# Optimization experiments

Measured on AMD Instinct MI355X. Metric: run time of the kernel, lower is better.

## Reference

```python
import jax, jax.numpy as jnp
from jax import lax
import numpy as np

N_WORDS, SENT_LEN, N_HEADS = 8192, 64, 1024
INPUT_SIZE, HIDDEN, DIST_EMB, CONV_CH, MAX_DIST = 768, 1024, 64, 4, 128
L_MAX = SENT_LEN  # static max sentence length (uniform sentences in setup)


def setup_inputs():
    key = jax.random.key(0)
    ks = jax.random.split(key, 8)
    sent_id = (jnp.arange(N_WORDS) // SENT_LEN).astype(jnp.int32)
    words = jax.random.normal(ks[0], (N_WORDS, INPUT_SIZE), jnp.float32)
    heads_ids = jnp.sort(jax.random.randint(ks[1], (N_HEADS,), 0, N_WORDS)).astype(jnp.int32)
    in_dim = 2 * INPUT_SIZE + DIST_EMB
    def lin(k, i, o):
        return (jax.random.normal(k, (i, o), jnp.float32) / np.float32(np.sqrt(i)))
    return dict(
        sent_id=sent_id, words=words, heads_ids=heads_ids,
        W1=lin(ks[2], in_dim, HIDDEN), b1=jnp.zeros((HIDDEN,), jnp.float32),
        W2=lin(ks[3], HIDDEN, 256), b2=jnp.zeros((256,), jnp.float32),
        W3=lin(ks[4], 256, DIST_EMB), b3=jnp.zeros((DIST_EMB,), jnp.float32),
        conv1_w=jax.random.normal(ks[5], (CONV_CH, DIST_EMB, 3), jnp.float32) * 0.05,
        conv1_b=jnp.zeros((CONV_CH,), jnp.float32),
        conv2_w=jax.random.normal(ks[6], (2, CONV_CH, 3), jnp.float32) * 0.2,
        conv2_b=jnp.zeros((2,), jnp.float32),
        emb=jax.random.normal(ks[7], (MAX_DIST, DIST_EMB), jnp.float32),
    )


def _conv1d(x, w, b):
    # x: [N, C_in, L], w: [C_out, C_in, K=3]; padding=1 exactly as the torch module
    y = lax.conv_general_dilated(x, w, (1,), [(1, 1)],
                                 dimension_numbers=('NCH', 'OIH', 'NCH'))
    return y + b[None, :, None]


def reference(sent_id, words, heads_ids, W1, b1, W2, b2, W3, b3,
              conv1_w, conv1_b, conv2_w, conv2_b, emb):
    n_words = words.shape[0]
    n_heads = heads_ids.shape[0]
    md = emb.shape[0]
    heads = heads_ids.astype(jnp.int32)
    sid_h = sent_id[heads]
    # sent_id is sorted: each sentence is a contiguous run of words, so the
    # ragged nonzero(same_sent) cols for head h are start[h] .. start[h]+len[h]-1
    start = jnp.searchsorted(sent_id, sid_h, side='left')
    lengths = jnp.searchsorted(sent_id, sid_h, side='right') - start
    j = jnp.arange(L_MAX)
    cols = start[:, None] + j[None, :]                  # [H, L]
    valid = j[None, :] < lengths[:, None]               # padding_mask
    cols_c = jnp.minimum(cols, n_words - 1)
    rel = heads[:, None] - cols_c                       # relative positions
    emb_ids = rel + (md - 2) // 2
    emb_ids = jnp.where((emb_ids < 0) | (emb_ids > md - 2), md - 1, emb_ids)
    # padded pair matrix: [H, L, 2*input + dist_emb], zeros at padded slots
    pair = jnp.concatenate([
        jnp.broadcast_to(words[heads][:, None, :], (n_heads, L_MAX, words.shape[1])),
        words[cols_c],
        emb[emb_ids],
    ], axis=-1)
    pair = jnp.where(valid[..., None], pair, 0.0)
    # FFNN (eval mode: dropout = identity)
    h = jax.nn.relu(pair @ W1 + b1)
    h = jax.nn.relu(h @ W2 + b2)
    h = h @ W3 + b3                                     # [H, L, DIST_EMB]
    x = jnp.transpose(h, (0, 2, 1))                     # [H, C, L]
    x = _conv1d(x, conv1_w, conv1_b)
    x = _conv1d(x, conv2_w, conv2_b)
    res = jnp.transpose(x, (0, 2, 1))                   # [H, L, 2]
    # scatter valid entries back into a -inf-filled [H, n_words, 2] tensor
    scores = jnp.full((n_heads, n_words, 2), -jnp.inf, jnp.float32)
    rows = jnp.broadcast_to(jnp.arange(n_heads)[:, None], cols.shape)
    cols_sc = jnp.where(valid, cols, n_words)           # OOB index -> dropped
    scores = scores.at[rows, cols_sc].set(res, mode='drop')
    # eval-mode validity masks: starts must be <= head, ends >= head
    rel_full = heads[:, None] - jnp.arange(n_words)[None, :]
    valid_starts = jnp.where(rel_full >= 0, 0.0, -jnp.inf)
    valid_ends = jnp.where(rel_full <= 0, 0.0, -jnp.inf)
    return scores + jnp.stack([valid_starts, valid_ends], axis=2)
```

## Files before the change

### kernel.cpp

```cpp
#include <hip/hip_runtime.h>
#include <cstdint>
#include <cstddef>

#define NW   8192
#define NH   1024
#define INP  768
#define HID  1024
#define DE   64
#define LMAX 64

#define NEG_SENT (-3.0e38f)

typedef short bf16x8 __attribute__((ext_vector_type(8)));
typedef float f32x4  __attribute__((ext_vector_type(4)));

__device__ __forceinline__ unsigned short f2bf(float f) {
    unsigned u = __builtin_bit_cast(unsigned, f);
    u += 0x7FFFu + ((u >> 16) & 1u);
    return (unsigned short)(u >> 16);
}
__device__ __forceinline__ float bcf(unsigned u) {
    return __builtin_bit_cast(float, u);
}

__device__ __forceinline__ void gload_lds16(const void* g, void* lds) {
    __builtin_amdgcn_global_load_lds(
        (const __attribute__((address_space(1))) unsigned int*)g,
        (__attribute__((address_space(3))) unsigned int*)lds, 16, 0, 0);
}

__device__ __forceinline__ bf16x8 mk_af(uint4 u, uint4 v, uint4 e) {
    bf16x8 r;
    const unsigned* up = (const unsigned*)&u;
    const unsigned* vp = (const unsigned*)&v;
    const unsigned* ep = (const unsigned*)&e;
    unsigned* rp = (unsigned*)&r;
    #pragma unroll
    for (int q = 0; q < 4; ++q) {
        const unsigned ud = up[q], vd = vp[q], ed = ep[q];
        float slo = bcf(ud << 16) + bcf(vd << 16) + bcf(ed << 16);
        float shi = bcf(ud & 0xffff0000u) + bcf(vd & 0xffff0000u) + bcf(ed & 0xffff0000u);
        slo = fmaxf(slo, 0.f);
        shi = fmaxf(shi, 0.f);
        rp[q] = (unsigned)f2bf(slo) | ((unsigned)f2bf(shi) << 16);
    }
    return r;
}

__device__ __forceinline__ void pack_frags_body(
    const float* __restrict__ src, uint4* __restrict__ dst,
    int Ntiles, int N, int t)
{
    const int frag = t >> 6, l = t & 63;
    const int kc = frag / Ntiles, nt = frag - kc * Ntiles;
    const int k0 = kc * 32 + ((l >> 4) << 3);
    const int n  = nt * 16 + (l & 15);
    unsigned wv[4];
    #pragma unroll
    for (int r = 0; r < 4; ++r) {
        const unsigned lo = f2bf(src[(size_t)(k0 + 2 * r)     * N + n]);
        const unsigned hi = f2bf(src[(size_t)(k0 + 2 * r + 1) * N + n]);
        wv[r] = lo | (hi << 16);
    }
    dst[t] = make_uint4(wv[0], wv[1], wv[2], wv[3]);
}

__device__ __forceinline__ void pack_rows_body(
    const float* __restrict__ src, uint4* __restrict__ dst,
    const int* __restrict__ gather, int Kc, int ldsrc, int t)
{
    const int l = t & 63, frag = t >> 6;
    const int mt = frag / Kc, kc = frag - mt * Kc;
    int row = mt * 16 + (l & 15);
    if (gather) row = gather[row];
    const int k0 = kc * 32 + ((l >> 4) << 3);
    const float* s = src + (size_t)row * ldsrc + k0;
    unsigned wv[4];
    #pragma unroll
    for (int r = 0; r < 4; ++r) {
        const unsigned lo = f2bf(s[2 * r]);
        const unsigned hi = f2bf(s[2 * r + 1]);
        wv[r] = lo | (hi << 16);
    }
    dst[t] = make_uint4(wv[0], wv[1], wv[2], wv[3]);
}

__global__ __launch_bounds__(256) void pack_all(
    const int* __restrict__ sent_id, const int* __restrict__ heads_ids,
    const float* __restrict__ W1, const float* __restrict__ b1,
    const float* __restrict__ W2, const float* __restrict__ W3,
    const float* __restrict__ words, const float* __restrict__ emb,
    uint4* __restrict__ W2p, uint4* __restrict__ W3p,
    uint4* __restrict__ W1bp, uint4* __restrict__ W1ap,
    uint4* __restrict__ W1cp, uint4* __restrict__ Ep_a,
    uint4* __restrict__ Awp, uint4* __restrict__ Aup,
    unsigned short* __restrict__ b1b, unsigned short* __restrict__ zrow,
    int* __restrict__ hstart, int* __restrict__ hlen)
{
    const int b = blockIdx.x, tid = threadIdx.x;
    if (b < 4) {
        const int i = b * 256 + tid;
        b1b[i] = f2bf(b1[i]);
        zrow[i] = 0;
        const int head = heads_ids[i];
        const int sid = sent_id[head];
        int lo = 0, hi = NW;
        while (lo < hi) { int m = (lo + hi) >> 1; if (sent_id[m] < sid) lo = m + 1; else hi = m; }
        const int st = lo;
        int lo2 = lo, hi2 = NW;
        while (lo2 < hi2) { int m = (lo2 + hi2) >> 1; if (sent_id[m] <= sid) lo2 = m + 1; else hi2 = m; }
        int ln = lo2 - st;
        if (ln > LMAX) ln = LMAX;
        hstart[i] = st; hlen[i] = ln;
    }
    else if (b < 132)  pack_frags_body(W2, W2p, 16, 256, (b - 4) * 256 + tid);
    else if (b < 140)  pack_frags_body(W3, W3p, 4, 64, (b - 132) * 256 + tid);
    else if (b < 524)  pack_frags_body(W1 + (size_t)INP * HID, W1bp, 64, 1024, (b - 140) * 256 + tid);
    else if (b < 908)  pack_frags_body(W1, W1ap, 64, 1024, (b - 524) * 256 + tid);
    else if (b < 940)  pack_frags_body(W1 + (size_t)2 * INP * HID, W1cp, 64, 1024, (b - 908) * 256 + tid);
    else if (b < 4012) pack_rows_body(words, Awp, nullptr, 24, INP, (b - 940) * 256 + tid);
    else if (b < 4396) pack_rows_body(words, Aup, heads_ids, 24, INP, (b - 4012) * 256 + tid);
    else               pack_rows_body(emb, Ep_a, nullptr, 2, DE, (b - 4396) * 256 + tid);
}

__global__ __launch_bounds__(256) void gemm_vue(
    const uint4* __restrict__ Awp, const uint4* __restrict__ W1bp,
    const uint4* __restrict__ Aup, const uint4* __restrict__ W1ap,
    const uint4* __restrict__ Ep_a, const uint4* __restrict__ W1cp,
    const float* __restrict__ b1,
    unsigned short* __restrict__ Vb, unsigned short* __restrict__ Ub,
    unsigned short* __restrict__ Eb)
{
    __shared__ uint4 sAB[2][1024];
    const int tid = threadIdx.x;
    const int l = tid & 63, wid = tid >> 6;

    const uint4 *Ap, *Bp;
    unsigned short* Cb;
    const float* bias = nullptr;
    int Kc, by, bx;
    {
        const int bid = blockIdx.x;
        if (bid < 512)      { Ap = Awp;  Bp = W1bp; Cb = Vb; Kc = 24; by = bid >> 3; bx = bid & 7; }
        else if (bid < 576) { const int bb = bid - 512; Ap = Aup; Bp = W1ap; Cb = Ub; bias = b1; Kc = 24; by = bb >> 3; bx = bb & 7; }
        else                { const int bb = bid - 576; Ap = Ep_a; Bp = W1cp; Cb = Eb; Kc = 2; by = 0; bx = bb; }
    }
    const int mt0 = by * 8, nt0 = bx * 8;
    const int NtTot = 64, N = 1024;
    const int wm = (wid >> 1) * 4, wn = (wid & 1) * 4;

    f32x4 acc[4][4];
    #pragma unroll
    for (int i = 0; i < 4; ++i)
        #pragma unroll
        for (int j = 0; j < 4; ++j) acc[i][j] = (f32x4){0.f, 0.f, 0.f, 0.f};

    #pragma unroll
    for (int i = 0; i < 2; ++i) {
        const int f = i * 4 + wid;
        gload_lds16(Ap + (size_t)(mt0 + f) * Kc * 64 + l, &sAB[0][f * 64 + l]);
        gload_lds16(Bp + (size_t)(nt0 + f) * 64 + l,      &sAB[0][(8 + f) * 64 + l]);
    }

    for (int kc = 0; kc < Kc; ++kc) {
        const int p = kc & 1;
        __builtin_amdgcn_s_barrier();
        if (kc + 1 < Kc) {
            #pragma unroll
            for (int i = 0; i < 2; ++i) {
                const int f = i * 4 + wid;
                gload_lds16(Ap + ((size_t)(mt0 + f) * Kc + kc + 1) * 64 + l,
                            &sAB[p ^ 1][f * 64 + l]);
                gload_lds16(Bp + ((size_t)(kc + 1) * NtTot + nt0 + f) * 64 + l,
                            &sAB[p ^ 1][(8 + f) * 64 + l]);
            }
            asm volatile("s_waitcnt vmcnt(4)" ::: "memory");
        } else {
            asm volatile("s_waitcnt vmcnt(0)" ::: "memory");
        }
        __builtin_amdgcn_s_barrier();
        bf16x8 af[4], bf[4];
        #pragma unroll
        for (int i = 0; i < 4; ++i)
            af[i] = *(const bf16x8*)&sAB[p][(wm + i) * 64 + l];
        #pragma unroll
        for (int j = 0; j < 4; ++j)
            bf[j] = *(const bf16x8*)&sAB[p][(8 + wn + j) * 64 + l];
        #pragma unroll
        for (int i = 0; i < 4; ++i)
            #pragma unroll
            for (int j = 0; j < 4; ++j)
                acc[i][j] = __builtin_amdgcn_mfma_f32_16x16x32_bf16(
                    af[i], bf[j], acc[i][j], 0, 0, 0);
    }
    const int bm = mt0 * 16, bn = nt0 * 16;
    #pragma unroll
    for (int i = 0; i < 4; ++i)
        #pragma unroll
        for (int j = 0; j < 4; ++j) {
            const int row0 = bm + (wm + i) * 16 + ((l >> 4) << 2);
            const int col  = bn + (wn + j) * 16 + (l & 15);
            const float bv = bias ? bias[col] : 0.f;
            #pragma unroll
            for (int r = 0; r < 4; ++r)
                Cb[(size_t)(row0 + r) * N + col] = f2bf(acc[i][j][r] + bv);
        }
}

__global__ __launch_bounds__(256, 3) void head_kernel(
    const int* __restrict__ hstart, const int* __restrict__ hlen,
    const int* __restrict__ heads_ids,
    const unsigned short* __restrict__ Vb, const unsigned short* __restrict__ Ub,
    const unsigned short* __restrict__ Eb, const unsigned short* __restrict__ b1b,
    const unsigned short* __restrict__ zrow,
    const uint4* __restrict__ W2p, const float* __restrict__ b2,
    const uint4* __restrict__ W3p, const float* __restrict__ b3,
    const float* __restrict__ c1w, const float* __restrict__ c1b,
    const float* __restrict__ c2w, const float* __restrict__ c2b,
    float* __restrict__ out)
{
    __shared__ char smem[50464];
    const int h   = blockIdx.x;
    const int tid = threadIdx.x;
    const int w = tid >> 6, l = tid & 63;
    const int head  = heads_ids[h];
    const int start = hstart[h];
    const int len   = hlen[h];

    const int arow = w * 16 + (l & 15);
    const int g8   = (l >> 4) << 3;
    const bool valid = arow < len;
    const int wglob = start + arow;
    const int wc    = wglob < NW ? wglob : NW - 1;
    int eid = head - wc + 63;
    eid = (eid < 0 || eid > 126) ? 127 : eid;
    const unsigned short* Up = valid ? Ub + (size_t)h   * HID : b1b;
    const unsigned short* Vp = valid ? Vb + (size_t)wc  * HID : zrow;
    const unsigned short* Ep = valid ? Eb + (size_t)eid * HID : zrow;

    char* slot0 = smem;
    char* slot1 = smem + 4096;
    char* myA   = smem + w * 1024 + l * 16;
    const uint4* WpB = W2p + (size_t)(w * 4) * 64 + l;

    f32x4 acc[16];
    #pragma unroll
    for (int i = 0; i < 16; ++i) acc[i] = (f32x4){0.f, 0.f, 0.f, 0.f};

    uint4 uA, vA, eA, uB, vB, eB;
    bf16x8 Ba0, Ba1, Ba2, Ba3, Bb0, Bb1, Bb2, Bb3;

    #define LOAD_AGL(kc, uu, vv, ee) do {                      \
        uu = *(const uint4*)(Up + (kc) * 32 + g8);             \
        vv = *(const uint4*)(Vp + (kc) * 32 + g8);             \
        ee = *(const uint4*)(Ep + (kc) * 32 + g8); } while (0)
    #define LOAD_B(kc, b0, b1v, b2v, b3v) do {                 \
        const uint4* p_ = WpB + (size_t)(kc) * 16 * 64;        \
        b0  = *(const bf16x8*)(p_);                            \
        b1v = *(const bf16x8*)(p_ + 64);                       \
        b2v = *(const bf16x8*)(p_ + 128);                      \
        b3v = *(const bf16x8*)(p_ + 192); } while (0)
    #define CONSUME(slot, b0, b1v, b2v, b3v) do {              \
        bf16x8 a0 = *(const bf16x8*)((slot) + 0 * 1024 + l * 16); \
        bf16x8 a1 = *(const bf16x8*)((slot) + 1 * 1024 + l * 16); \
        bf16x8 a2 = *(const bf16x8*)((slot) + 2 * 1024 + l * 16); \
        bf16x8 a3 = *(const bf16x8*)((slot) + 3 * 1024 + l * 16); \
        acc[0]  = __builtin_amdgcn_mfma_f32_16x16x32_bf16(a0, b0,  acc[0],  0,0,0); \
        acc[1]  = __builtin_amdgcn_mfma_f32_16x16x32_bf16(a0, b1v, acc[1],  0,0,0); \
        acc[2]  = __builtin_amdgcn_mfma_f32_16x16x32_bf16(a0, b2v, acc[2],  0,0,0); \
        acc[3]  = __builtin_amdgcn_mfma_f32_16x16x32_bf16(a0, b3v, acc[3],  0,0,0); \
        acc[4]  = __builtin_amdgcn_mfma_f32_16x16x32_bf16(a1, b0,  acc[4],  0,0,0); \
        acc[5]  = __builtin_amdgcn_mfma_f32_16x16x32_bf16(a1, b1v, acc[5],  0,0,0); \
        acc[6]  = __builtin_amdgcn_mfma_f32_16x16x32_bf16(a1, b2v, acc[6],  0,0,0); \
        acc[7]  = __builtin_amdgcn_mfma_f32_16x16x32_bf16(a1, b3v, acc[7],  0,0,0); \
        acc[8]  = __builtin_amdgcn_mfma_f32_16x16x32_bf16(a2, b0,  acc[8],  0,0,0); \
        acc[9]  = __builtin_amdgcn_mfma_f32_16x16x32_bf16(a2, b1v, acc[9],  0,0,0); \
        acc[10] = __builtin_amdgcn_mfma_f32_16x16x32_bf16(a2, b2v, acc[10], 0,0,0); \
        acc[11] = __builtin_amdgcn_mfma_f32_16x16x32_bf16(a2, b3v, acc[11], 0,0,0); \
        acc[12] = __builtin_amdgcn_mfma_f32_16x16x32_bf16(a3, b0,  acc[12], 0,0,0); \
        acc[13] = __builtin_amdgcn_mfma_f32_16x16x32_bf16(a3, b1v, acc[13], 0,0,0); \
        acc[14] = __builtin_amdgcn_mfma_f32_16x16x32_bf16(a3, b2v, acc[14], 0,0,0); \
        acc[15] = __builtin_amdgcn_mfma_f32_16x16x32_bf16(a3, b3v, acc[15], 0,0,0); } while (0)

    LOAD_AGL(0, uA, vA, eA);
    LOAD_B(0, Ba0, Ba1, Ba2, Ba3);
    LOAD_AGL(1, uB, vB, eB);
    LOAD_B(1, Bb0, Bb1, Bb2, Bb3);
    {
        bf16x8 af = mk_af(uA, vA, eA);
        *(bf16x8*)(slot0 + w * 1024 + l * 16) = af;
    }
    LOAD_AGL(2, uA, vA, eA);

    for (int kc = 0; kc < 32; kc += 2) {
        __builtin_amdgcn_s_barrier();
        {
            bf16x8 af = mk_af(uB, vB, eB);
            *(bf16x8*)(slot1 + w * 1024 + l * 16) = af;
        }
        if (kc + 3 < 32) LOAD_AGL(kc + 3, uB, vB, eB);
        CONSUME(slot0, Ba0, Ba1, Ba2, Ba3);
        if (kc + 2 < 32) LOAD_B(kc + 2, Ba0, Ba1, Ba2, Ba3);
        __builtin_amdgcn_s_barrier();
        if (kc + 2 < 32) {
            bf16x8 af = mk_af(uA, vA, eA);
            *(bf16x8*)(slot0 + w * 1024 + l * 16) = af;
        }
        if (kc + 4 < 32) LOAD_AGL(kc + 4, uA, vA, eA);
        CONSUME(slot1, Bb0, Bb1, Bb2, Bb3);
        if (kc + 3 < 32) LOAD_B(kc + 3, Bb0, Bb1, Bb2, Bb3);
    }
    #undef LOAD_AGL
    #undef LOAD_B
    #undef CONSUME
    (void)myA;

    __syncthreads();
    {
        float b2v[4];
        #pragma unroll
        for (int ntl = 0; ntl < 4; ++ntl) b2v[ntl] = b2[w * 64 + ntl * 16 + (l & 15)];
        #pragma unroll
        for (int mt = 0; mt < 4; ++mt)
            #pragma unroll
            for (int ntl = 0; ntl < 4; ++ntl) {
                const int n = w * 64 + ntl * 16 + (l & 15);
                #pragma unroll
                for (int r = 0; r < 4; ++r) {
                    const int m = mt * 16 + ((l >> 4) << 2) + r;
                    const float x = fmaxf(acc[mt * 4 + ntl][r] + b2v[ntl], 0.f);
                    *(unsigned short*)(smem + m * 512 + ((n * 2) ^ ((m & 7) << 4))) = f2bf(x);
                }
            }
    }
    __syncthreads();

    f32x4 acc3[4];
    #pragma unroll
    for (int i = 0; i < 4; ++i) acc3[i] = (f32x4){0.f, 0.f, 0.f, 0.f};
    const int mrow = w * 16 + (l & 15);
    #pragma unroll
    for (int kc = 0; kc < 8; ++kc) {
        const int n0 = kc * 32 + g8;
        const bf16x8 af = *(const bf16x8*)(smem + mrow * 512 + ((n0 * 2) ^ ((mrow & 7) << 4)));
        #pragma unroll
        for (int nt = 0; nt < 4; ++nt) {
            const bf16x8 bf = *(const bf16x8*)(W3p + (size_t)((kc << 2) + nt) * 64 + l);
            acc3[nt] = __builtin_amdgcn_mfma_f32_16x16x32_bf16(af, bf, acc3[nt], 0, 0, 0);
        }
    }
    float* h3s = (float*)(smem + 32768);
    float* o1  = (float*)(smem + 32768 + 16640);
    #pragma unroll
    for (int nt = 0; nt < 4; ++nt) {
        const int c = nt * 16 + (l & 15);
        const float b3v = b3[c];
        #pragma unroll
        for (int r = 0; r < 4; ++r) {
            const int m = w * 16 + ((l >> 4) << 2) + r;
            h3s[m * 65 + c] = acc3[nt][r] + b3v;
        }
    }
    if (tid < 8) o1[(tid >> 1) * 66 + ((tid & 1) ? 65 : 0)] = 0.f;
    __syncthreads();

    {
        const int o = tid >> 6, ll = tid & 63;
        float a = c1b[o];
        #pragma unroll 8
        for (int cc = 0; cc < 64; ++cc) {
            const float w0  = c1w[o * 192 + cc * 3 + 0];
            const float w1  = c1w[o * 192 + cc * 3 + 1];
            const float w2v = c1w[o * 192 + cc * 3 + 2];
            if (ll > 0)  a += h3s[(ll - 1) * 65 + cc] * w0;
            a += h3s[ll * 65 + cc] * w1;
            if (ll < 63) a += h3s[(ll + 1) * 65 + cc] * w2v;
        }
        o1[o * 66 + ll + 1] = a;
    }
    __syncthreads();

    if (tid < 128) {
        const int s = tid >> 6, ll = tid & 63;
        float z = c2b[s];
        #pragma unroll
        for (int cc = 0; cc < 4; ++cc)
            #pragma unroll
            for (int k = 0; k < 3; ++k)
                z += o1[cc * 66 + ll + k] * c2w[s * 12 + cc * 3 + k];
        if (ll < len) {
            const int wv = start + ll;
            const bool ok = (s == 0) ? (wv <= head) : (wv >= head);
            out[(size_t)h * (NW * 2) + (size_t)wv * 2 + s] = ok ? z : NEG_SENT;
        }
    }

    {
        float4 ni; ni.x = NEG_SENT; ni.y = NEG_SENT; ni.z = NEG_SENT; ni.w = NEG_SENT;
        float4* orow = reinterpret_cast<float4*>(out + (size_t)h * (NW * 2));
        const int cA = start >> 1;
        const int cB = (start + len - 1) >> 1;
        for (int ch = tid; ch < NW / 2; ch += 256) {
            if (ch >= cA && ch <= cB) {
                #pragma unroll
                for (int t = 0; t < 2; ++t) {
                    const int wv = 2 * ch + t;
                    if (wv < start || wv >= start + len) {
                        out[(size_t)h * (NW * 2) + (size_t)wv * 2]     = NEG_SENT;
                        out[(size_t)h * (NW * 2) + (size_t)wv * 2 + 1] = NEG_SENT;
                    }
                }
            } else {
                orow[ch] = ni;
            }
        }
    }
}

extern "C" void kernel_launch(void* const* d_in, const int* in_sizes, int n_in,
                              void* d_out, int out_size, void* d_ws, size_t ws_size,
                              hipStream_t stream)
{
    const int*   sent_id = (const int*)  d_in[0];
    const float* words   = (const float*)d_in[1];
    const int*   heads   = (const int*)  d_in[2];
    const float* W1      = (const float*)d_in[3];
    const float* b1      = (const float*)d_in[4];
    const float* W2      = (const float*)d_in[5];
    const float* b2      = (const float*)d_in[6];
    const float* W3      = (const float*)d_in[7];
    const float* b3      = (const float*)d_in[8];
    const float* c1w     = (const float*)d_in[9];
    const float* c1b     = (const float*)d_in[10];
    const float* c2w     = (const float*)d_in[11];
    const float* c2b     = (const float*)d_in[12];
    const float* emb     = (const float*)d_in[13];
    float* out = (float*)d_out;

    uint4* W2p  = (uint4*)d_ws;
    uint4* W3p  = W2p  + 32 * 16 * 64;
    uint4* W1bp = W3p  + 8 * 4 * 64;
    uint4* W1ap = W1bp + 24 * 64 * 64;
    uint4* W1cp = W1ap + 24 * 64 * 64;
    uint4* Ep_a = W1cp + 2 * 64 * 64;
    uint4* Awp  = Ep_a + 8 * 2 * 64;
    uint4* Aup  = Awp  + 512 * 24 * 64;
    unsigned short* Vb   = (unsigned short*)(Aup + 64 * 24 * 64);
    unsigned short* Ub   = Vb + (size_t)NW * HID;
    unsigned short* Eb   = Ub + (size_t)NH * HID;
    unsigned short* b1b  = Eb + (size_t)128 * HID;
    unsigned short* zrow = b1b + HID;
    int* hstart = (int*)(zrow + HID);
    int* hlen   = hstart + NH;

    dim3 blk(256);
    pack_all<<<dim3(4400), blk, 0, stream>>>(
        sent_id, heads, W1, b1, W2, W3, words, emb,
        W2p, W3p, W1bp, W1ap, W1cp, Ep_a, Awp, Aup, b1b, zrow, hstart, hlen);
    gemm_vue<<<dim3(584), blk, 0, stream>>>(
        Awp, W1bp, Aup, W1ap, Ep_a, W1cp, b1, Vb, Ub, Eb);
    head_kernel<<<dim3(NH), blk, 0, stream>>>(
        hstart, hlen, heads, Vb, Ub, Eb, b1b, zrow,
        W2p, b2, W3p, b3, c1w, c1b, c2w, c2b, out);
}
```

Before: 234.8 us.

## Fuse activation bf16 packing into GEMM and shrink head kernel LDS

```diff
diff --git a/kernel.cpp b/kernel.cpp
--- a/kernel.cpp
+++ b/kernel.cpp
@@ -44,6 +44,15 @@
         shi = fmaxf(shi, 0.f);
         rp[q] = (unsigned)f2bf(slo) | ((unsigned)f2bf(shi) << 16);
     }
+    return r;
+}
+
+__device__ __forceinline__ bf16x8 cvt8(float4 x, float4 y) {
+    bf16x8 r;
+    r[0] = (short)f2bf(x.x); r[1] = (short)f2bf(x.y);
+    r[2] = (short)f2bf(x.z); r[3] = (short)f2bf(x.w);
+    r[4] = (short)f2bf(y.x); r[5] = (short)f2bf(y.y);
+    r[6] = (short)f2bf(y.z); r[7] = (short)f2bf(y.w);
     return r;
 }
 
@@ -65,35 +74,13 @@
     dst[t] = make_uint4(wv[0], wv[1], wv[2], wv[3]);
 }
 
-__device__ __forceinline__ void pack_rows_body(
-    const float* __restrict__ src, uint4* __restrict__ dst,
-    const int* __restrict__ gather, int Kc, int ldsrc, int t)
-{
-    const int l = t & 63, frag = t >> 6;
-    const int mt = frag / Kc, kc = frag - mt * Kc;
-    int row = mt * 16 + (l & 15);
-    if (gather) row = gather[row];
-    const int k0 = kc * 32 + ((l >> 4) << 3);
-    const float* s = src + (size_t)row * ldsrc + k0;
-    unsigned wv[4];
-    #pragma unroll
-    for (int r = 0; r < 4; ++r) {
-        const unsigned lo = f2bf(s[2 * r]);
-        const unsigned hi = f2bf(s[2 * r + 1]);
-        wv[r] = lo | (hi << 16);
-    }
-    dst[t] = make_uint4(wv[0], wv[1], wv[2], wv[3]);
-}
-
 __global__ __launch_bounds__(256) void pack_all(
     const int* __restrict__ sent_id, const int* __restrict__ heads_ids,
     const float* __restrict__ W1, const float* __restrict__ b1,
     const float* __restrict__ W2, const float* __restrict__ W3,
-    const float* __restrict__ words, const float* __restrict__ emb,
     uint4* __restrict__ W2p, uint4* __restrict__ W3p,
     uint4* __restrict__ W1bp, uint4* __restrict__ W1ap,
-    uint4* __restrict__ W1cp, uint4* __restrict__ Ep_a,
-    uint4* __restrict__ Awp, uint4* __restrict__ Aup,
+    uint4* __restrict__ W1cp,
     unsigned short* __restrict__ b1b, unsigned short* __restrict__ zrow,
     int* __restrict__ hstart, int* __restrict__ hlen)
 {
@@ -117,75 +104,89 @@
     else if (b < 140)  pack_frags_body(W3, W3p, 4, 64, (b - 132) * 256 + tid);
     else if (b < 524)  pack_frags_body(W1 + (size_t)INP * HID, W1bp, 64, 1024, (b - 140) * 256 + tid);
     else if (b < 908)  pack_frags_body(W1, W1ap, 64, 1024, (b - 524) * 256 + tid);
-    else if (b < 940)  pack_frags_body(W1 + (size_t)2 * INP * HID, W1cp, 64, 1024, (b - 908) * 256 + tid);
-    else if (b < 4012) pack_rows_body(words, Awp, nullptr, 24, INP, (b - 940) * 256 + tid);
-    else if (b < 4396) pack_rows_body(words, Aup, heads_ids, 24, INP, (b - 4012) * 256 + tid);
-    else               pack_rows_body(emb, Ep_a, nullptr, 2, DE, (b - 4396) * 256 + tid);
+    else               pack_frags_body(W1 + (size_t)2 * INP * HID, W1cp, 64, 1024, (b - 908) * 256 + tid);
 }
 
 __global__ __launch_bounds__(256) void gemm_vue(
-    const uint4* __restrict__ Awp, const uint4* __restrict__ W1bp,
-    const uint4* __restrict__ Aup, const uint4* __restrict__ W1ap,
-    const uint4* __restrict__ Ep_a, const uint4* __restrict__ W1cp,
-    const float* __restrict__ b1,
+    const float* __restrict__ words, const int* __restrict__ heads_ids,
+    const float* __restrict__ emb,
+    const uint4* __restrict__ W1bp, const uint4* __restrict__ W1ap,
+    const uint4* __restrict__ W1cp, const float* __restrict__ b1,
     unsigned short* __restrict__ Vb, unsigned short* __restrict__ Ub,
     unsigned short* __restrict__ Eb)
 {
-    __shared__ uint4 sAB[2][1024];
+    __shared__ char sbuf[2][16384];
     const int tid = threadIdx.x;
     const int l = tid & 63, wid = tid >> 6;
 
-    const uint4 *Ap, *Bp;
-    unsigned short* Cb;
-    const float* bias = nullptr;
-    int Kc, by, bx;
+    const float* Asrc; const int* gather = nullptr;
+    const uint4* Bp; unsigned short* Cb; const float* bias = nullptr;
+    int Kc, by, bx, lda;
     {
         const int bid = blockIdx.x;
-        if (bid < 512)      { Ap = Awp;  Bp = W1bp; Cb = Vb; Kc = 24; by = bid >> 3; bx = bid & 7; }
-        else if (bid < 576) { const int bb = bid - 512; Ap = Aup; Bp = W1ap; Cb = Ub; bias = b1; Kc = 24; by = bb >> 3; bx = bb & 7; }
-        else                { const int bb = bid - 576; Ap = Ep_a; Bp = W1cp; Cb = Eb; Kc = 2; by = 0; bx = bb; }
+        if (bid < 512)      { Asrc = words; lda = INP; Bp = W1bp; Cb = Vb; Kc = 24; by = bid >> 3; bx = bid & 7; }
+        else if (bid < 576) { const int bb = bid - 512; Asrc = words; lda = INP; gather = heads_ids; Bp = W1ap; Cb = Ub; bias = b1; Kc = 24; by = bb >> 3; bx = bb & 7; }
+        else                { const int bb = bid - 576; Asrc = emb; lda = DE; Bp = W1cp; Cb = Eb; Kc = 2; by = 0; bx = bb; }
     }
     const int mt0 = by * 8, nt0 = bx * 8;
     const int NtTot = 64, N = 1024;
     const int wm = (wid >> 1) * 4, wn = (wid & 1) * 4;
 
+    const float* arow[2]; int koffA[2];
+    #pragma unroll
+    for (int q = 0; q < 2; ++q) {
+        const int e = tid + q * 256;
+        const int f = e >> 6, ll2 = e & 63;
+        int r = (mt0 + f) * 16 + (ll2 & 15);
+        if (gather) r = gather[r];
+        arow[q]  = Asrc + (size_t)r * lda;
+        koffA[q] = (ll2 >> 4) << 3;
+    }
+
     f32x4 acc[4][4];
     #pragma unroll
     for (int i = 0; i < 4; ++i)
         #pragma unroll
         for (int j = 0; j < 4; ++j) acc[i][j] = (f32x4){0.f, 0.f, 0.f, 0.f};
 
-    #pragma unroll
-    for (int i = 0; i < 2; ++i) {
-        const int f = i * 4 + wid;
-        gload_lds16(Ap + (size_t)(mt0 + f) * Kc * 64 + l, &sAB[0][f * 64 + l]);
-        gload_lds16(Bp + (size_t)(nt0 + f) * 64 + l,      &sAB[0][(8 + f) * 64 + l]);
-    }
+    float4 a0, a1, a2, a3;
+    #define STAGE_A_LOAD(kc) do {                                          \
+        a0 = *(const float4*)(arow[0] + (kc) * 32 + koffA[0]);             \
+        a1 = *(const float4*)(arow[0] + (kc) * 32 + koffA[0] + 4);         \
+        a2 = *(const float4*)(arow[1] + (kc) * 32 + koffA[1]);             \
+        a3 = *(const float4*)(arow[1] + (kc) * 32 + koffA[1] + 4); } while (0)
+    #define STAGE_B(kc, b) do {                                            \
+        gload_lds16(Bp + ((size_t)(kc) * NtTot + nt0 + wid) * 64 + l,      \
+                    sbuf[b] + 8192 + wid * 1024 + l * 16);                 \
+        gload_lds16(Bp + ((size_t)(kc) * NtTot + nt0 + 4 + wid) * 64 + l,  \
+                    sbuf[b] + 8192 + (4 + wid) * 1024 + l * 16); } while (0)
+    #define STAGE_A_WRITE(b) do {                                          \
+        *(bf16x8*)(sbuf[b] + tid * 16)         = cvt8(a0, a1);             \
+        *(bf16x8*)(sbuf[b] + (tid + 256) * 16) = cvt8(a2, a3); } while (0)
+
+    STAGE_A_LOAD(0);
+    STAGE_B(0, 0);
+    STAGE_A_WRITE(0);
 
     for (int kc = 0; kc < Kc; ++kc) {
         const int p = kc & 1;
         __builtin_amdgcn_s_barrier();
         if (kc + 1 < Kc) {
-            #pragma unroll
-            for (int i = 0; i < 2; ++i) {
-                const int f = i * 4 + wid;
-                gload_lds16(Ap + ((size_t)(mt0 + f) * Kc + kc + 1) * 64 + l,
-                            &sAB[p ^ 1][f * 64 + l]);
-                gload_lds16(Bp + ((size_t)(kc + 1) * NtTot + nt0 + f) * 64 + l,
-                            &sAB[p ^ 1][(8 + f) * 64 + l]);
-            }
-            asm volatile("s_waitcnt vmcnt(4)" ::: "memory");
+            STAGE_A_LOAD(kc + 1);
+            STAGE_B(kc + 1, p ^ 1);
+            STAGE_A_WRITE(p ^ 1);
+            asm volatile("s_waitcnt vmcnt(2) lgkmcnt(0)" ::: "memory");
         } else {
-            asm volatile("s_waitcnt vmcnt(0)" ::: "memory");
+            asm volatile("s_waitcnt vmcnt(0) lgkmcnt(0)" ::: "memory");
         }
         __builtin_amdgcn_s_barrier();
         bf16x8 af[4], bf[4];
         #pragma unroll
         for (int i = 0; i < 4; ++i)
-            af[i] = *(const bf16x8*)&sAB[p][(wm + i) * 64 + l];
+            af[i] = *(const bf16x8*)(sbuf[p] + ((wm + i) * 64 + l) * 16);
         #pragma unroll
         for (int j = 0; j < 4; ++j)
-            bf[j] = *(const bf16x8*)&sAB[p][(8 + wn + j) * 64 + l];
+            bf[j] = *(const bf16x8*)(sbuf[p] + 8192 + ((wn + j) * 64 + l) * 16);
         #pragma unroll
         for (int i = 0; i < 4; ++i)
             #pragma unroll
@@ -193,6 +194,10 @@
                 acc[i][j] = __builtin_amdgcn_mfma_f32_16x16x32_bf16(
                     af[i], bf[j], acc[i][j], 0, 0, 0);
     }
+    #undef STAGE_A_LOAD
+    #undef STAGE_B
+    #undef STAGE_A_WRITE
+
     const int bm = mt0 * 16, bn = nt0 * 16;
     #pragma unroll
     for (int i = 0; i < 4; ++i)
@@ -207,7 +212,7 @@
         }
 }
 
-__global__ __launch_bounds__(256, 3) void head_kernel(
+__global__ __launch_bounds__(256, 4) void head_kernel(
     const int* __restrict__ hstart, const int* __restrict__ hlen,
     const int* __restrict__ heads_ids,
     const unsigned short* __restrict__ Vb, const unsigned short* __restrict__ Ub,
@@ -219,8 +224,8 @@
     const float* __restrict__ c2w, const float* __restrict__ c2b,
     float* __restrict__ out)
 {
-    __shared__ char smem[50464];
-    const int h   = blockIdx.x;
+    __shared__ char smem[32768];
+    const int h   = (blockIdx.x & 7) * 128 + (blockIdx.x >> 3);
     const int tid = threadIdx.x;
     const int w = tid >> 6, l = tid & 63;
     const int head  = heads_ids[h];
@@ -240,7 +245,6 @@
 
     char* slot0 = smem;
     char* slot1 = smem + 4096;
-    char* myA   = smem + w * 1024 + l * 16;
     const uint4* WpB = W2p + (size_t)(w * 4) * 64 + l;
 
     f32x4 acc[16];
@@ -313,7 +317,6 @@
     #undef LOAD_AGL
     #undef LOAD_B
     #undef CONSUME
-    (void)myA;
 
     __syncthreads();
     {
@@ -349,8 +352,9 @@
             acc3[nt] = __builtin_amdgcn_mfma_f32_16x16x32_bf16(af, bf, acc3[nt], 0, 0, 0);
         }
     }
-    float* h3s = (float*)(smem + 32768);
-    float* o1  = (float*)(smem + 32768 + 16640);
+    __syncthreads();
+    float* h3s = (float*)smem;
+    float* o1  = (float*)(smem + 16640);
     #pragma unroll
     for (int nt = 0; nt < 4; ++nt) {
         const int c = nt * 16 + (l & 15);
@@ -442,10 +446,7 @@
     uint4* W1bp = W3p  + 8 * 4 * 64;
     uint4* W1ap = W1bp + 24 * 64 * 64;
     uint4* W1cp = W1ap + 24 * 64 * 64;
-    uint4* Ep_a = W1cp + 2 * 64 * 64;
-    uint4* Awp  = Ep_a + 8 * 2 * 64;
-    uint4* Aup  = Awp  + 512 * 24 * 64;
-    unsigned short* Vb   = (unsigned short*)(Aup + 64 * 24 * 64);
+    unsigned short* Vb   = (unsigned short*)(W1cp + 2 * 64 * 64);
     unsigned short* Ub   = Vb + (size_t)NW * HID;
     unsigned short* Eb   = Ub + (size_t)NH * HID;
     unsigned short* b1b  = Eb + (size_t)128 * HID;
@@ -454,11 +455,11 @@
     int* hlen   = hstart + NH;
 
     dim3 blk(256);
-    pack_all<<<dim3(4400), blk, 0, stream>>>(
-        sent_id, heads, W1, b1, W2, W3, words, emb,
-        W2p, W3p, W1bp, W1ap, W1cp, Ep_a, Awp, Aup, b1b, zrow, hstart, hlen);
+    pack_all<<<dim3(940), blk, 0, stream>>>(
+        sent_id, heads, W1, b1, W2, W3,
+        W2p, W3p, W1bp, W1ap, W1cp, b1b, zrow, hstart, hlen);
     gemm_vue<<<dim3(584), blk, 0, stream>>>(
-        Awp, W1bp, Aup, W1ap, Ep_a, W1cp, b1, Vb, Ub, Eb);
+        words, heads, emb, W1bp, W1ap, W1cp, b1, Vb, Ub, Eb);
     head_kernel<<<dim3(NH), blk, 0, stream>>>(
         hstart, hlen, heads, Vb, Ub, Eb, b1b, zrow,
         W2p, b2, W3p, b3, c1w, c1b, c2w, c2b, out);
```

Measured after the change: 349.6 us. +48.9%, slower.
